# Performance work log

Measured on AMD Instinct MI355X. Metric: run time of the kernel, lower is better.

The kernel has to match this reference:

```python
import jax, jax.numpy as jnp
import numpy as np

N_NODES = 20000
N_EDGES = 320000
IN_F = 256
HID = 64
OUT_F = 64
EDGE_F = 16
HEADS = 4
NUM_CLASSES = 10
NUM_GRAPHS = 40
ALPHA = 0.2  # LeakyReLU negative slope


def _xavier(key, shape):
    fan_in, fan_out = shape[0], shape[-1]
    std = 1.414 * np.sqrt(2.0 / (fan_in + fan_out))
    return jax.random.normal(key, shape, dtype=jnp.float32) * std


def setup_inputs() -> dict:
    key = jax.random.key(0)
    ks = jax.random.split(key, 12)
    x = jax.random.normal(ks[0], (N_NODES, IN_F), dtype=jnp.float32)
    edge_index = jax.random.randint(ks[1], (2, N_EDGES), 0, N_NODES, dtype=jnp.int32)
    edge_attr = jax.random.uniform(ks[2], (N_EDGES, EDGE_F), dtype=jnp.float32)
    batch = jnp.sort(jax.random.randint(ks[3], (N_NODES,), 0, NUM_GRAPHS, dtype=jnp.int32))
    # layer 0: in=IN_F, heads=HEADS, out=HID, concat
    W0 = _xavier(ks[4], (IN_F, HEADS * HID))
    a0 = _xavier(ks[5], (HEADS, 2 * HID + EDGE_F))
    # layer 1: in=HID*HEADS, heads=HEADS, out=HID, concat
    W1 = _xavier(ks[6], (HID * HEADS, HEADS * HID))
    a1 = _xavier(ks[7], (HEADS, 2 * HID + EDGE_F))
    # layer 2: in=HID*HEADS, heads=1, out=OUT_F, mean over heads
    W2 = _xavier(ks[8], (HID * HEADS, 1 * OUT_F))
    a2 = _xavier(ks[9], (1, 2 * OUT_F + EDGE_F))
    cls_w = _xavier(ks[10], (OUT_F, NUM_CLASSES))
    cls_b = jnp.zeros((NUM_CLASSES,), dtype=jnp.float32)
    return {"x": x, "edge_index": edge_index, "edge_attr": edge_attr, "batch": batch,
            "W0": W0, "a0": a0, "W1": W1, "a1": a1, "W2": W2, "a2": a2,
            "cls_w": cls_w, "cls_b": cls_b}


def gat_layer(h, W, a, edge_index, edge_attr, heads, out_f, concat):
    n = h.shape[0]
    Wh = (h @ W).reshape(n, heads, out_f)              # [N,H,D]
    src, dst = edge_index[0], edge_index[1]
    a_i, a_j, a_e = a[:, :out_f], a[:, out_f:2 * out_f], a[:, 2 * out_f:]
    # per-node head scores, gathered per edge (equivalent to concat + dot with a)
    s_i = jnp.einsum('nhd,hd->nh', Wh, a_i)            # [N,H]
    s_j = jnp.einsum('nhd,hd->nh', Wh, a_j)            # [N,H]
    s_e = edge_attr @ a_e.T                            # [E,H]
    e = s_i[src] + s_j[dst] + s_e                      # [E,H]
    e = jnp.where(e > 0, e, ALPHA * e)                 # LeakyReLU
    # NB: faithful to source — softmax over the HEADS dim (dim=1), not per-node
    att = jax.nn.softmax(e, axis=1)                    # [E,H]
    msg = att[:, :, None] * Wh[dst]                    # [E,H,D]
    h_prime = jax.ops.segment_sum(msg, src, num_segments=n)  # scatter-add to src
    if concat:
        return jax.nn.elu(h_prime.reshape(n, heads * out_f))
    return h_prime.mean(axis=1)


def reference(x, edge_index, edge_attr, batch, W0, a0, W1, a1, W2, a2, cls_w, cls_b):
    h = gat_layer(x, W0, a0, edge_index, edge_attr, HEADS, HID, True)
    h = gat_layer(h, W1, a1, edge_index, edge_attr, HEADS, HID, True)
    h = gat_layer(h, W2, a2, edge_index, edge_attr, 1, OUT_F, False)
    # global mean pool over graphs
    sums = jax.ops.segment_sum(h, batch, num_segments=NUM_GRAPHS)
    cnts = jax.ops.segment_sum(jnp.ones((h.shape[0],), h.dtype), batch, num_segments=NUM_GRAPHS)
    pooled = sums / jnp.maximum(cnts, 1.0)[:, None]
    logits = pooled @ cls_w + cls_b
    return jax.nn.log_softmax(logits, axis=1)
```

## Files before the change

### kernel.cpp

```cpp
#include <hip/hip_runtime.h>
#include <hip/hip_bf16.h>
#include <math.h>

#define N_NODES 20000
#define N_EDGES 320000
#define IN_F 256
#define HID 64
#define HEADS 4
#define OUT_F 64
#define EDGE_F 16
#define NUM_CLASSES 10
#define NUM_GRAPHS 40
#define LRELU_ALPHA 0.2f

typedef short bf16x8 __attribute__((ext_vector_type(8)));
typedef unsigned short u16x8 __attribute__((ext_vector_type(8)));
typedef float f32x4 __attribute__((ext_vector_type(4)));

static __device__ __forceinline__ float bf2f(unsigned short u) {
    union { unsigned int i; float f; } v; v.i = ((unsigned int)u) << 16; return v.f;
}
static __device__ __forceinline__ unsigned short f2bf(float f) {
    union { float f; unsigned int i; } v; v.f = f;
    unsigned int r = v.i + 0x7FFF + ((v.i >> 16) & 1);
    return (unsigned short)(r >> 16);
}
static __device__ __forceinline__ float eluf(float a) {
    return a > 0.f ? a : __expf(a) - 1.0f;
}

__global__ void wconv_kernel(const float* __restrict__ W0, const float* __restrict__ W1,
                             const float* __restrict__ W2, unsigned short* __restrict__ W0b,
                             unsigned short* __restrict__ W1b, unsigned short* __restrict__ W2b) {
    int i = blockIdx.x * blockDim.x + threadIdx.x;
    const float* src; unsigned short* dst; int off;
    if (i < 16384)      { src = W0; dst = W0b; off = i; }
    else if (i < 32768) { src = W1; dst = W1b; off = i - 16384; }
    else if (i < 36864) { src = W2; dst = W2b; off = i - 32768; }
    else return;
    float4 v = ((const float4*)src)[off];
    ushort4 o;
    o.x = f2bf(v.x); o.y = f2bf(v.y); o.z = f2bf(v.z); o.w = f2bf(v.w);
    ((ushort4*)dst)[off] = o;
}

__global__ void count_kernel(const int* __restrict__ src, int* __restrict__ cnt) {
    int e = blockIdx.x * blockDim.x + threadIdx.x;
    if (e < N_EDGES) atomicAdd(&cnt[src[e]], 1);
}

__global__ __launch_bounds__(1024) void scan_kernel(const int* __restrict__ cnt,
                                                    int* __restrict__ row_ptr,
                                                    int* __restrict__ cursor) {
    __shared__ int wsum[16];
    __shared__ int carry_s;
    int t = threadIdx.x;
    int lane = t & 63, wave = t >> 6;
    if (t == 0) { carry_s = 0; row_ptr[0] = 0; }
    __syncthreads();
    for (int base = 0; base < N_NODES; base += 1024) {
        int idx = base + t;
        int x0 = (idx < N_NODES) ? cnt[idx] : 0;
        int x = x0;
#pragma unroll
        for (int off = 1; off < 64; off <<= 1) {
            int y = __shfl_up(x, off, 64);
            if (lane >= off) x += y;
        }
        if (lane == 63) wsum[wave] = x;
        __syncthreads();
        if (wave == 0 && lane < 16) {
            int s = wsum[lane];
#pragma unroll
            for (int off = 1; off < 16; off <<= 1) {
                int y = __shfl_up(s, off, 64);
                if (lane >= off) s += y;
            }
            wsum[lane] = s;
        }
        __syncthreads();
        int waveoff = (wave > 0) ? wsum[wave - 1] : 0;
        int carry = carry_s;
        if (idx < N_NODES) {
            int incl = x + waveoff + carry;
            row_ptr[idx + 1] = incl;
            cursor[idx] = incl - x0;
        }
        __syncthreads();
        if (t == 0) carry_s = carry + wsum[15];
        __syncthreads();
    }
}

__global__ void scatter_kernel(const int* __restrict__ src, const int* __restrict__ dst,
                               const float* __restrict__ ea, int* __restrict__ cursor,
                               int* __restrict__ srcp, int* __restrict__ dstp,
                               float* __restrict__ eap) {
    int e = blockIdx.x * blockDim.x + threadIdx.x;
    if (e < N_EDGES) {
        int s = src[e];
        int pos = atomicAdd(&cursor[s], 1);
        srcp[pos] = s;
        dstp[pos] = dst[e];
#pragma unroll
        for (int k = 0; k < 4; ++k)
            ((float4*)(eap + (size_t)pos * 16))[k] = ((const float4*)(ea + (size_t)e * 16))[k];
    }
}

template <bool AF32, bool SCORES>
__global__ __launch_bounds__(256) void gemm_bf16(const void* __restrict__ Aptr,
                                                 const unsigned short* __restrict__ B,
                                                 unsigned short* __restrict__ C,
                                                 const float* __restrict__ avec,
                                                 float* __restrict__ si, float* __restrict__ sj,
                                                 int M, int N, int K) {
    __shared__ unsigned short As[64][40];
    __shared__ unsigned short Bs[64][40];
    __shared__ unsigned short Cs[64][72];
    __shared__ float sa[128];
    int tid = threadIdx.x;
    if (SCORES && tid < 128) sa[tid] = avec[blockIdx.y * 144 + tid];
    int bm = blockIdx.x * 64, bn = blockIdx.y * 64;
    int w = tid >> 6, l = tid & 63;
    int wr = (w >> 1) * 32, wc = (w & 1) * 32;
    int lr = l & 15, lk = (l >> 4) * 8;
    f32x4 acc[2][2] = {};
    int ar = tid >> 2, akc = (tid & 3) * 8;
    int bk = tid >> 3, bn8 = tid & 7, bnc = bn8 * 8;

    for (int k0 = 0; k0 < K; k0 += 32) {
        bf16x8 av = {};
        if (bm + ar < M) {
            if constexpr (AF32) {
                const float* Af = (const float*)Aptr + (size_t)(bm + ar) * K + k0 + akc;
                float4 f0 = *(const float4*)Af;
                float4 f1 = *(const float4*)(Af + 4);
                av[0] = (short)f2bf(f0.x); av[1] = (short)f2bf(f0.y);
                av[2] = (short)f2bf(f0.z); av[3] = (short)f2bf(f0.w);
                av[4] = (short)f2bf(f1.x); av[5] = (short)f2bf(f1.y);
                av[6] = (short)f2bf(f1.z); av[7] = (short)f2bf(f1.w);
            } else {
                av = *(const bf16x8*)((const unsigned short*)Aptr + (size_t)(bm + ar) * K + k0 + akc);
            }
        }
        *(bf16x8*)&As[ar][akc] = av;
        bf16x8 bv = *(const bf16x8*)(B + (size_t)(k0 + bk) * N + bn + bnc);
#pragma unroll
        for (int j = 0; j < 8; ++j) {
            int jj = (j + bn8) & 7;
            Bs[bnc + jj][bk] = (unsigned short)bv[jj];
        }
        __syncthreads();
        bf16x8 a0 = *(const bf16x8*)&As[wr + lr][lk];
        bf16x8 a1 = *(const bf16x8*)&As[wr + 16 + lr][lk];
        bf16x8 b0 = *(const bf16x8*)&Bs[wc + lr][lk];
        bf16x8 b1 = *(const bf16x8*)&Bs[wc + 16 + lr][lk];
        acc[0][0] = __builtin_amdgcn_mfma_f32_16x16x32_bf16(a0, b0, acc[0][0], 0, 0, 0);
        acc[0][1] = __builtin_amdgcn_mfma_f32_16x16x32_bf16(a0, b1, acc[0][1], 0, 0, 0);
        acc[1][0] = __builtin_amdgcn_mfma_f32_16x16x32_bf16(a1, b0, acc[1][0], 0, 0, 0);
        acc[1][1] = __builtin_amdgcn_mfma_f32_16x16x32_bf16(a1, b1, acc[1][1], 0, 0, 0);
        __syncthreads();
    }
#pragma unroll
    for (int i = 0; i < 2; ++i)
#pragma unroll
        for (int j = 0; j < 2; ++j)
#pragma unroll
            for (int r = 0; r < 4; ++r)
                Cs[wr + i * 16 + (l >> 4) * 4 + r][wc + j * 16 + (l & 15)] = f2bf(acc[i][j][r]);
    __syncthreads();
    int row = tid >> 3, cc = (tid & 7) * 8;
#pragma unroll
    for (int p = 0; p < 2; ++p, row += 32) {
        if (bm + row < M) {
            bf16x8 o = *(const bf16x8*)&Cs[row][cc];
            *(bf16x8*)(C + (size_t)(bm + row) * N + bn + cc) = o;
        }
    }
    if (SCORES) {
        int r = tid >> 2, qq = tid & 3;
        float s0 = 0.f, s1 = 0.f;
#pragma unroll
        for (int k = 0; k < 16; ++k) {
            float f = bf2f(Cs[r][qq * 16 + k]);
            s0 += f * sa[qq * 16 + k];
            s1 += f * sa[64 + qq * 16 + k];
        }
        s0 += __shfl_xor(s0, 1, 64); s0 += __shfl_xor(s0, 2, 64);
        s1 += __shfl_xor(s1, 1, 64); s1 += __shfl_xor(s1, 2, 64);
        if (qq == 0 && bm + r < M) {
            si[(size_t)(bm + r) * 4 + blockIdx.y] = s0;
            sj[(size_t)(bm + r) * 4 + blockIdx.y] = s1;
        }
    }
}

__global__ void att_kernel(const int* __restrict__ srcp, const int* __restrict__ dstp,
                           const float* __restrict__ eap, const float* __restrict__ a,
                           const float* __restrict__ si, const float* __restrict__ sj,
                           float* __restrict__ attp) {
    __shared__ float ae[HEADS][EDGE_F];
    int tid = threadIdx.x;
    if (tid < HEADS * EDGE_F) ae[tid >> 4][tid & 15] = a[(tid >> 4) * 144 + 128 + (tid & 15)];
    __syncthreads();
    int i = blockIdx.x * blockDim.x + tid;
    if (i >= N_EDGES) return;
    int s = srcp[i], u = dstp[i];
    float4 siv = ((const float4*)si)[s];
    float4 sjv = ((const float4*)sj)[u];
    float x[16];
#pragma unroll
    for (int k = 0; k < 16; k += 4) {
        float4 v = *(const float4*)(eap + (size_t)i * 16 + k);
        x[k] = v.x; x[k + 1] = v.y; x[k + 2] = v.z; x[k + 3] = v.w;
    }
    float se0 = 0.f, se1 = 0.f, se2 = 0.f, se3 = 0.f;
#pragma unroll
    for (int k = 0; k < 16; ++k) {
        se0 += x[k] * ae[0][k];
        se1 += x[k] * ae[1][k];
        se2 += x[k] * ae[2][k];
        se3 += x[k] * ae[3][k];
    }
    float t0 = siv.x + sjv.x + se0;
    float t1 = siv.y + sjv.y + se1;
    float t2 = siv.z + sjv.z + se2;
    float t3 = siv.w + sjv.w + se3;
    t0 = t0 > 0.f ? t0 : LRELU_ALPHA * t0;
    t1 = t1 > 0.f ? t1 : LRELU_ALPHA * t1;
    t2 = t2 > 0.f ? t2 : LRELU_ALPHA * t2;
    t3 = t3 > 0.f ? t3 : LRELU_ALPHA * t3;
    float m = fmaxf(fmaxf(t0, t1), fmaxf(t2, t3));
    float p0 = __expf(t0 - m), p1 = __expf(t1 - m), p2 = __expf(t2 - m), p3 = __expf(t3 - m);
    float inv = 1.0f / (p0 + p1 + p2 + p3);
    ((float4*)attp)[i] = make_float4(p0 * inv, p1 * inv, p2 * inv, p3 * inv);
}

__global__ __launch_bounds__(256) void edge_agg_concat(
    const unsigned short* __restrict__ Whb, const float* __restrict__ attp,
    const int* __restrict__ row_ptr, const int* __restrict__ dstp,
    unsigned short* __restrict__ out) {
    int v = blockIdx.x * 4 + (threadIdx.x >> 6);
    if (v >= N_NODES) return;
    int l = threadIdx.x & 63;
    int slot = l >> 4, p = l & 15;
    int beg = row_ptr[v], end = row_ptr[v + 1];
    float acc0[8] = {}, acc1[8] = {};
    int i = beg + slot;
    int u_n = 0;
    float4 at_n = make_float4(0.f, 0.f, 0.f, 0.f);
    if (i < end) { u_n = dstp[i]; at_n = ((const float4*)attp)[i]; }
    for (; i < end; i += 4) {
        int u = u_n;
        float4 at4 = at_n;
        if (i + 4 < end) { u_n = dstp[i + 4]; at_n = ((const float4*)attp)[i + 4]; }
        const unsigned short* row = Whb + (size_t)u * 256;
        u16x8 w0 = *(const u16x8*)(row + p * 8);
        u16x8 w1 = *(const u16x8*)(row + 128 + p * 8);
        float atA = (p & 8) ? at4.y : at4.x;
        float atB = (p & 8) ? at4.w : at4.z;
#pragma unroll
        for (int j = 0; j < 8; ++j) acc0[j] += atA * bf2f(w0[j]);
#pragma unroll
        for (int j = 0; j < 8; ++j) acc1[j] += atB * bf2f(w1[j]);
    }
#pragma unroll
    for (int j = 0; j < 8; ++j) {
        acc0[j] += __shfl_xor(acc0[j], 16, 64);
        acc0[j] += __shfl_xor(acc0[j], 32, 64);
        acc1[j] += __shfl_xor(acc1[j], 16, 64);
        acc1[j] += __shfl_xor(acc1[j], 32, 64);
    }
    if (slot == 0) {
        u16x8 o0, o1;
#pragma unroll
        for (int j = 0; j < 8; ++j) {
            o0[j] = f2bf(eluf(acc0[j]));
            o1[j] = f2bf(eluf(acc1[j]));
        }
        *(u16x8*)(out + (size_t)v * 256 + p * 8) = o0;
        *(u16x8*)(out + (size_t)v * 256 + 128 + p * 8) = o1;
    }
}

__global__ __launch_bounds__(256) void edge_agg_single(
    const unsigned short* __restrict__ Whb, const int* __restrict__ row_ptr,
    const int* __restrict__ dstp, float* __restrict__ out) {
    int v = blockIdx.x * 4 + (threadIdx.x >> 6);
    if (v >= N_NODES) return;
    int l = threadIdx.x & 63;
    int slot = l >> 3, p = l & 7;
    int beg = row_ptr[v], end = row_ptr[v + 1];
    float acc[8] = {};
    int i = beg + slot;
    int u_n = 0;
    if (i < end) u_n = dstp[i];
    for (; i < end; i += 8) {
        int u = u_n;
        if (i + 8 < end) u_n = dstp[i + 8];
        u16x8 w = *(const u16x8*)(Whb + (size_t)u * 64 + p * 8);
#pragma unroll
        for (int j = 0; j < 8; ++j) acc[j] += bf2f(w[j]);
    }
#pragma unroll
    for (int j = 0; j < 8; ++j) {
        acc[j] += __shfl_xor(acc[j], 8, 64);
        acc[j] += __shfl_xor(acc[j], 16, 64);
        acc[j] += __shfl_xor(acc[j], 32, 64);
    }
    if (l < 8) {
        float4 o0 = make_float4(acc[0], acc[1], acc[2], acc[3]);
        float4 o1 = make_float4(acc[4], acc[5], acc[6], acc[7]);
        *(float4*)(out + (size_t)v * 64 + p * 8) = o0;
        *(float4*)(out + (size_t)v * 64 + p * 8 + 4) = o1;
    }
}

__global__ __launch_bounds__(1024) void pool_kernel(const float* __restrict__ h3,
                                                    const int* __restrict__ batch,
                                                    float* __restrict__ pooled) {
    int g = blockIdx.x;
    int lane = threadIdx.x & 63;
    int wave = threadIdx.x >> 6;
    int lo = 0, hi = N_NODES;
    while (lo < hi) { int mid = (lo + hi) >> 1; if (batch[mid] < g) lo = mid + 1; else hi = mid; }
    int start = lo;
    lo = start; hi = N_NODES;
    while (lo < hi) { int mid = (lo + hi) >> 1; if (batch[mid] < g + 1) lo = mid + 1; else hi = mid; }
    int endi = lo;
    float s = 0.f;
    for (int v = start + wave; v < endi; v += 16) s += h3[(size_t)v * 64 + lane];
    __shared__ float red[16][64];
    red[wave][lane] = s;
    __syncthreads();
    if (wave == 0) {
        float t = red[0][lane];
#pragma unroll
        for (int w = 1; w < 16; ++w) t += red[w][lane];
        float c = (float)((endi - start) > 1 ? (endi - start) : 1);
        pooled[g * 64 + lane] = t / c;
    }
}

__global__ void classify_kernel(const float* __restrict__ pooled, const float* __restrict__ cw,
                                const float* __restrict__ cb, float* __restrict__ out) {
    int g = threadIdx.x;
    if (g >= NUM_GRAPHS) return;
    float lg[NUM_CLASSES];
#pragma unroll
    for (int c = 0; c < NUM_CLASSES; ++c) lg[c] = cb[c];
    for (int d = 0; d < OUT_F; ++d) {
        float p = pooled[g * 64 + d];
#pragma unroll
        for (int c = 0; c < NUM_CLASSES; ++c) lg[c] += p * cw[d * NUM_CLASSES + c];
    }
    float m = lg[0];
#pragma unroll
    for (int c = 1; c < NUM_CLASSES; ++c) m = fmaxf(m, lg[c]);
    float s = 0.f;
#pragma unroll
    for (int c = 0; c < NUM_CLASSES; ++c) s += expf(lg[c] - m);
    float lse = m + logf(s);
#pragma unroll
    for (int c = 0; c < NUM_CLASSES; ++c) out[g * NUM_CLASSES + c] = lg[c] - lse;
}

extern "C" void kernel_launch(void* const* d_in, const int* in_sizes, int n_in,
                              void* d_out, int out_size, void* d_ws, size_t ws_size,
                              hipStream_t stream) {
    const float* x   = (const float*)d_in[0];
    const int*   ei  = (const int*)d_in[1];
    const float* ea  = (const float*)d_in[2];
    const int* batch = (const int*)d_in[3];
    const float* W0  = (const float*)d_in[4];
    const float* a0  = (const float*)d_in[5];
    const float* W1  = (const float*)d_in[6];
    const float* a1  = (const float*)d_in[7];
    const float* W2  = (const float*)d_in[8];
    const float* cw  = (const float*)d_in[10];
    const float* cb  = (const float*)d_in[11];
    float* out = (float*)d_out;

    const int* srcg = ei;
    const int* dstg = ei + N_EDGES;

    char* ws = (char*)d_ws;
    size_t off = 0;
    auto alloc = [&](size_t bytes) -> char* {
        char* p = ws + off;
        off += (bytes + 255) & ~(size_t)255;
        return p;
    };
    unsigned short* W0b  = (unsigned short*)alloc(256 * 256 * 2);
    unsigned short* W1b  = (unsigned short*)alloc(256 * 256 * 2);
    unsigned short* W2b  = (unsigned short*)alloc(256 * 64 * 2);
    unsigned short* Whb  = (unsigned short*)alloc((size_t)N_NODES * 256 * 2);
    unsigned short* hAb  = (unsigned short*)alloc((size_t)N_NODES * 256 * 2);
    unsigned short* hBb  = (unsigned short*)alloc((size_t)N_NODES * 256 * 2);
    unsigned short* Wh2b = (unsigned short*)alloc((size_t)N_NODES * 64 * 2);
    float* si   = (float*)alloc((size_t)N_NODES * HEADS * 4);
    float* sj   = (float*)alloc((size_t)N_NODES * HEADS * 4);
    float* attp = (float*)alloc((size_t)N_EDGES * HEADS * 4);
    float* eap  = (float*)alloc((size_t)N_EDGES * EDGE_F * 4);
    int* row_ptr = (int*)alloc((N_NODES + 1) * 4);
    int* cursor  = (int*)alloc(N_NODES * 4);
    int* cnt  = (int*)alloc(N_NODES * 4);
    int* srcp = (int*)alloc(N_EDGES * 4);
    int* dstp = (int*)alloc(N_EDGES * 4);
    float* h3 = (float*)alloc((size_t)N_NODES * 64 * 4);
    float* pooled = (float*)alloc(NUM_GRAPHS * 64 * 4);

    wconv_kernel<<<144, 256, 0, stream>>>(W0, W1, W2, W0b, W1b, W2b);

    hipMemsetAsync(cnt, 0, N_NODES * 4, stream);
    count_kernel<<<(N_EDGES + 255) / 256, 256, 0, stream>>>(srcg, cnt);
    scan_kernel<<<1, 1024, 0, stream>>>(cnt, row_ptr, cursor);
    scatter_kernel<<<(N_EDGES + 255) / 256, 256, 0, stream>>>(srcg, dstg, ea, cursor,
                                                              srcp, dstp, eap);

    dim3 ggrid((N_NODES + 63) / 64, 4);
    dim3 ggrid2((N_NODES + 63) / 64, 1);
    int atb = (N_EDGES + 255) / 256;
    int agb = (N_NODES + 3) / 4;

    gemm_bf16<true, true><<<ggrid, 256, 0, stream>>>(x, W0b, Whb, a0, si, sj, N_NODES, 256, 256);
    att_kernel<<<atb, 256, 0, stream>>>(srcp, dstp, eap, a0, si, sj, attp);
    edge_agg_concat<<<agb, 256, 0, stream>>>(Whb, attp, row_ptr, dstp, hAb);

    gemm_bf16<false, true><<<ggrid, 256, 0, stream>>>(hAb, W1b, Whb, a1, si, sj, N_NODES, 256, 256);
    att_kernel<<<atb, 256, 0, stream>>>(srcp, dstp, eap, a1, si, sj, attp);
    edge_agg_concat<<<agb, 256, 0, stream>>>(Whb, attp, row_ptr, dstp, hBb);

    gemm_bf16<false, false><<<ggrid2, 256, 0, stream>>>(hBb, W2b, Wh2b, nullptr, nullptr, nullptr,
                                                        N_NODES, 64, 256);
    edge_agg_single<<<agb, 256, 0, stream>>>(Wh2b, row_ptr, dstp, h3);

    pool_kernel<<<NUM_GRAPHS, 1024, 0, stream>>>(h3, batch, pooled);
    classify_kernel<<<1, 64, 0, stream>>>(pooled, cw, cb, out);
}
```

Baseline: 209.3 us.

## Fuse attention into edge aggregation, precompute edge scores, enlarge GEMM tile

The separate attention kernel is removed. Edge-feature scores for both layers are computed once in the scatter pass and stored per edge as four floats. The LeakyReLU and head softmax are computed inline inside edge_agg_concat. This drops the 16-float permuted edge-attribute buffer, the srcp array and two kernel launches. Separately, the GEMM tile grows to 128 rows with each wave covering all 64 columns, and the count memset is folded into the weight-conversion kernel. The risks are fewer GEMM blocks and an extra dependent gather of sj per edge in the aggregation loop.

```diff
diff --git a/kernel.cpp b/kernel.cpp
--- a/kernel.cpp
+++ b/kernel.cpp
@@ -29,19 +29,25 @@
     return a > 0.f ? a : __expf(a) - 1.0f;
 }
 
-__global__ void wconv_kernel(const float* __restrict__ W0, const float* __restrict__ W1,
-                             const float* __restrict__ W2, unsigned short* __restrict__ W0b,
-                             unsigned short* __restrict__ W1b, unsigned short* __restrict__ W2b) {
-    int i = blockIdx.x * blockDim.x + threadIdx.x;
-    const float* src; unsigned short* dst; int off;
-    if (i < 16384)      { src = W0; dst = W0b; off = i; }
-    else if (i < 32768) { src = W1; dst = W1b; off = i - 16384; }
-    else if (i < 36864) { src = W2; dst = W2b; off = i - 32768; }
-    else return;
-    float4 v = ((const float4*)src)[off];
-    ushort4 o;
-    o.x = f2bf(v.x); o.y = f2bf(v.y); o.z = f2bf(v.z); o.w = f2bf(v.w);
-    ((ushort4*)dst)[off] = o;
+__global__ void prep_kernel(const float* __restrict__ W0, const float* __restrict__ W1,
+                            const float* __restrict__ W2, unsigned short* __restrict__ W0b,
+                            unsigned short* __restrict__ W1b, unsigned short* __restrict__ W2b,
+                            int* __restrict__ cnt) {
+    int b = blockIdx.x;
+    if (b < 144) {
+        int i = b * 256 + threadIdx.x;
+        const float* src; unsigned short* dst; int off;
+        if (i < 16384)      { src = W0; dst = W0b; off = i; }
+        else if (i < 32768) { src = W1; dst = W1b; off = i - 16384; }
+        else                { src = W2; dst = W2b; off = i - 32768; }
+        float4 v = ((const float4*)src)[off];
+        ushort4 o;
+        o.x = f2bf(v.x); o.y = f2bf(v.y); o.z = f2bf(v.z); o.w = f2bf(v.w);
+        ((ushort4*)dst)[off] = o;
+    } else {
+        int j = (b - 144) * 256 + threadIdx.x;
+        if (j < N_NODES / 4) ((int4*)cnt)[j] = make_int4(0, 0, 0, 0);
+    }
 }
 
 __global__ void count_kernel(const int* __restrict__ src, int* __restrict__ cnt) {
@@ -93,19 +99,36 @@
 }
 
 __global__ void scatter_kernel(const int* __restrict__ src, const int* __restrict__ dst,
-                               const float* __restrict__ ea, int* __restrict__ cursor,
-                               int* __restrict__ srcp, int* __restrict__ dstp,
-                               float* __restrict__ eap) {
-    int e = blockIdx.x * blockDim.x + threadIdx.x;
-    if (e < N_EDGES) {
-        int s = src[e];
-        int pos = atomicAdd(&cursor[s], 1);
-        srcp[pos] = s;
-        dstp[pos] = dst[e];
-#pragma unroll
-        for (int k = 0; k < 4; ++k)
-            ((float4*)(eap + (size_t)pos * 16))[k] = ((const float4*)(ea + (size_t)e * 16))[k];
-    }
+                               const float* __restrict__ ea, const float* __restrict__ a0,
+                               const float* __restrict__ a1, int* __restrict__ cursor,
+                               int* __restrict__ dstp, float* __restrict__ se0,
+                               float* __restrict__ se1) {
+    __shared__ float ae[2][4][16];
+    int tid = threadIdx.x;
+    if (tid < 64) ae[0][tid >> 4][tid & 15] = a0[(tid >> 4) * 144 + 128 + (tid & 15)];
+    else if (tid < 128) { int t = tid - 64; ae[1][t >> 4][t & 15] = a1[(t >> 4) * 144 + 128 + (t & 15)]; }
+    __syncthreads();
+    int e = blockIdx.x * blockDim.x + tid;
+    if (e >= N_EDGES) return;
+    int s = src[e];
+    int pos = atomicAdd(&cursor[s], 1);
+    dstp[pos] = dst[e];
+    float x[16];
+#pragma unroll
+    for (int k = 0; k < 16; k += 4) {
+        float4 v = *(const float4*)(ea + (size_t)e * 16 + k);
+        x[k] = v.x; x[k + 1] = v.y; x[k + 2] = v.z; x[k + 3] = v.w;
+    }
+    float4 o0 = make_float4(0.f, 0.f, 0.f, 0.f), o1 = o0;
+#pragma unroll
+    for (int k = 0; k < 16; ++k) {
+        o0.x += x[k] * ae[0][0][k]; o0.y += x[k] * ae[0][1][k];
+        o0.z += x[k] * ae[0][2][k]; o0.w += x[k] * ae[0][3][k];
+        o1.x += x[k] * ae[1][0][k]; o1.y += x[k] * ae[1][1][k];
+        o1.z += x[k] * ae[1][2][k]; o1.w += x[k] * ae[1][3][k];
+    }
+    ((float4*)se0)[pos] = o0;
+    ((float4*)se1)[pos] = o1;
 }
 
 template <bool AF32, bool SCORES>
@@ -115,36 +138,45 @@
                                                  const float* __restrict__ avec,
                                                  float* __restrict__ si, float* __restrict__ sj,
                                                  int M, int N, int K) {
-    __shared__ unsigned short As[64][40];
+    __shared__ unsigned short As[128][40];
     __shared__ unsigned short Bs[64][40];
-    __shared__ unsigned short Cs[64][72];
+    __shared__ unsigned short Cs[128][72];
     __shared__ float sa[128];
     int tid = threadIdx.x;
     if (SCORES && tid < 128) sa[tid] = avec[blockIdx.y * 144 + tid];
-    int bm = blockIdx.x * 64, bn = blockIdx.y * 64;
+    int bm = blockIdx.x * 128, bn = blockIdx.y * 64;
     int w = tid >> 6, l = tid & 63;
-    int wr = (w >> 1) * 32, wc = (w & 1) * 32;
+    int wr = w * 32;
     int lr = l & 15, lk = (l >> 4) * 8;
-    f32x4 acc[2][2] = {};
-    int ar = tid >> 2, akc = (tid & 3) * 8;
+    f32x4 acc[2][4] = {};
+    int ar = tid >> 1, akc = (tid & 1) * 16;
     int bk = tid >> 3, bn8 = tid & 7, bnc = bn8 * 8;
 
     for (int k0 = 0; k0 < K; k0 += 32) {
-        bf16x8 av = {};
+        bf16x8 av0 = {}, av1 = {};
         if (bm + ar < M) {
             if constexpr (AF32) {
                 const float* Af = (const float*)Aptr + (size_t)(bm + ar) * K + k0 + akc;
-                float4 f0 = *(const float4*)Af;
-                float4 f1 = *(const float4*)(Af + 4);
-                av[0] = (short)f2bf(f0.x); av[1] = (short)f2bf(f0.y);
-                av[2] = (short)f2bf(f0.z); av[3] = (short)f2bf(f0.w);
-                av[4] = (short)f2bf(f1.x); av[5] = (short)f2bf(f1.y);
-                av[6] = (short)f2bf(f1.z); av[7] = (short)f2bf(f1.w);
+                float4 f0 = ((const float4*)Af)[0];
+                float4 f1 = ((const float4*)Af)[1];
+                float4 f2 = ((const float4*)Af)[2];
+                float4 f3 = ((const float4*)Af)[3];
+                av0[0] = (short)f2bf(f0.x); av0[1] = (short)f2bf(f0.y);
+                av0[2] = (short)f2bf(f0.z); av0[3] = (short)f2bf(f0.w);
+                av0[4] = (short)f2bf(f1.x); av0[5] = (short)f2bf(f1.y);
+                av0[6] = (short)f2bf(f1.z); av0[7] = (short)f2bf(f1.w);
+                av1[0] = (short)f2bf(f2.x); av1[1] = (short)f2bf(f2.y);
+                av1[2] = (short)f2bf(f2.z); av1[3] = (short)f2bf(f2.w);
+                av1[4] = (short)f2bf(f3.x); av1[5] = (short)f2bf(f3.y);
+                av1[6] = (short)f2bf(f3.z); av1[7] = (short)f2bf(f3.w);
             } else {
-                av = *(const bf16x8*)((const unsigned short*)Aptr + (size_t)(bm + ar) * K + k0 + akc);
+                const unsigned short* Ab = (const unsigned short*)Aptr + (size_t)(bm + ar) * K + k0 + akc;
+                av0 = *(const bf16x8*)Ab;
+                av1 = *(const bf16x8*)(Ab + 8);
             }
         }
-        *(bf16x8*)&As[ar][akc] = av;
+        *(bf16x8*)&As[ar][akc] = av0;
+        *(bf16x8*)&As[ar][akc + 8] = av1;
         bf16x8 bv = *(const bf16x8*)(B + (size_t)(k0 + bk) * N + bn + bnc);
 #pragma unroll
         for (int j = 0; j < 8; ++j) {
@@ -154,91 +186,59 @@
         __syncthreads();
         bf16x8 a0 = *(const bf16x8*)&As[wr + lr][lk];
         bf16x8 a1 = *(const bf16x8*)&As[wr + 16 + lr][lk];
-        bf16x8 b0 = *(const bf16x8*)&Bs[wc + lr][lk];
-        bf16x8 b1 = *(const bf16x8*)&Bs[wc + 16 + lr][lk];
+        bf16x8 b0 = *(const bf16x8*)&Bs[lr][lk];
+        bf16x8 b1 = *(const bf16x8*)&Bs[16 + lr][lk];
+        bf16x8 b2 = *(const bf16x8*)&Bs[32 + lr][lk];
+        bf16x8 b3 = *(const bf16x8*)&Bs[48 + lr][lk];
         acc[0][0] = __builtin_amdgcn_mfma_f32_16x16x32_bf16(a0, b0, acc[0][0], 0, 0, 0);
         acc[0][1] = __builtin_amdgcn_mfma_f32_16x16x32_bf16(a0, b1, acc[0][1], 0, 0, 0);
+        acc[0][2] = __builtin_amdgcn_mfma_f32_16x16x32_bf16(a0, b2, acc[0][2], 0, 0, 0);
+        acc[0][3] = __builtin_amdgcn_mfma_f32_16x16x32_bf16(a0, b3, acc[0][3], 0, 0, 0);
         acc[1][0] = __builtin_amdgcn_mfma_f32_16x16x32_bf16(a1, b0, acc[1][0], 0, 0, 0);
         acc[1][1] = __builtin_amdgcn_mfma_f32_16x16x32_bf16(a1, b1, acc[1][1], 0, 0, 0);
+        acc[1][2] = __builtin_amdgcn_mfma_f32_16x16x32_bf16(a1, b2, acc[1][2], 0, 0, 0);
+        acc[1][3] = __builtin_amdgcn_mfma_f32_16x16x32_bf16(a1, b3, acc[1][3], 0, 0, 0);
         __syncthreads();
     }
 #pragma unroll
     for (int i = 0; i < 2; ++i)
 #pragma unroll
-        for (int j = 0; j < 2; ++j)
+        for (int j = 0; j < 4; ++j)
 #pragma unroll
             for (int r = 0; r < 4; ++r)
-                Cs[wr + i * 16 + (l >> 4) * 4 + r][wc + j * 16 + (l & 15)] = f2bf(acc[i][j][r]);
+                Cs[wr + i * 16 + (l >> 4) * 4 + r][j * 16 + (l & 15)] = f2bf(acc[i][j][r]);
     __syncthreads();
-    int row = tid >> 3, cc = (tid & 7) * 8;
-#pragma unroll
-    for (int p = 0; p < 2; ++p, row += 32) {
-        if (bm + row < M) {
-            bf16x8 o = *(const bf16x8*)&Cs[row][cc];
-            *(bf16x8*)(C + (size_t)(bm + row) * N + bn + cc) = o;
+    {
+        int row = tid >> 3, cc = (tid & 7) * 8;
+#pragma unroll
+        for (int p = 0; p < 4; ++p, row += 32) {
+            if (bm + row < M) {
+                bf16x8 o = *(const bf16x8*)&Cs[row][cc];
+                *(bf16x8*)(C + (size_t)(bm + row) * N + bn + cc) = o;
+            }
         }
     }
     if (SCORES) {
-        int r = tid >> 2, qq = tid & 3;
+        int r = tid >> 1, half = tid & 1;
         float s0 = 0.f, s1 = 0.f;
 #pragma unroll
-        for (int k = 0; k < 16; ++k) {
-            float f = bf2f(Cs[r][qq * 16 + k]);
-            s0 += f * sa[qq * 16 + k];
-            s1 += f * sa[64 + qq * 16 + k];
-        }
-        s0 += __shfl_xor(s0, 1, 64); s0 += __shfl_xor(s0, 2, 64);
-        s1 += __shfl_xor(s1, 1, 64); s1 += __shfl_xor(s1, 2, 64);
-        if (qq == 0 && bm + r < M) {
+        for (int k = 0; k < 32; ++k) {
+            float f = bf2f(Cs[r][half * 32 + k]);
+            s0 += f * sa[half * 32 + k];
+            s1 += f * sa[64 + half * 32 + k];
+        }
+        s0 += __shfl_xor(s0, 1, 64);
+        s1 += __shfl_xor(s1, 1, 64);
+        if (half == 0 && bm + r < M) {
             si[(size_t)(bm + r) * 4 + blockIdx.y] = s0;
             sj[(size_t)(bm + r) * 4 + blockIdx.y] = s1;
         }
     }
 }
 
-__global__ void att_kernel(const int* __restrict__ srcp, const int* __restrict__ dstp,
-                           const float* __restrict__ eap, const float* __restrict__ a,
-                           const float* __restrict__ si, const float* __restrict__ sj,
-                           float* __restrict__ attp) {
-    __shared__ float ae[HEADS][EDGE_F];
-    int tid = threadIdx.x;
-    if (tid < HEADS * EDGE_F) ae[tid >> 4][tid & 15] = a[(tid >> 4) * 144 + 128 + (tid & 15)];
-    __syncthreads();
-    int i = blockIdx.x * blockDim.x + tid;
-    if (i >= N_EDGES) return;
-    int s = srcp[i], u = dstp[i];
-    float4 siv = ((const float4*)si)[s];
-    float4 sjv = ((const float4*)sj)[u];
-    float x[16];
-#pragma unroll
-    for (int k = 0; k < 16; k += 4) {
-        float4 v = *(const float4*)(eap + (size_t)i * 16 + k);
-        x[k] = v.x; x[k + 1] = v.y; x[k + 2] = v.z; x[k + 3] = v.w;
-    }
-    float se0 = 0.f, se1 = 0.f, se2 = 0.f, se3 = 0.f;
-#pragma unroll
-    for (int k = 0; k < 16; ++k) {
-        se0 += x[k] * ae[0][k];
-        se1 += x[k] * ae[1][k];
-        se2 += x[k] * ae[2][k];
-        se3 += x[k] * ae[3][k];
-    }
-    float t0 = siv.x + sjv.x + se0;
-    float t1 = siv.y + sjv.y + se1;
-    float t2 = siv.z + sjv.z + se2;
-    float t3 = siv.w + sjv.w + se3;
-    t0 = t0 > 0.f ? t0 : LRELU_ALPHA * t0;
-    t1 = t1 > 0.f ? t1 : LRELU_ALPHA * t1;
-    t2 = t2 > 0.f ? t2 : LRELU_ALPHA * t2;
-    t3 = t3 > 0.f ? t3 : LRELU_ALPHA * t3;
-    float m = fmaxf(fmaxf(t0, t1), fmaxf(t2, t3));
-    float p0 = __expf(t0 - m), p1 = __expf(t1 - m), p2 = __expf(t2 - m), p3 = __expf(t3 - m);
-    float inv = 1.0f / (p0 + p1 + p2 + p3);
-    ((float4*)attp)[i] = make_float4(p0 * inv, p1 * inv, p2 * inv, p3 * inv);
-}
-
 __global__ __launch_bounds__(256) void edge_agg_concat(
-    const unsigned short* __restrict__ Whb, const float* __restrict__ attp,
+    const unsigned short* __restrict__ Whb, const float* __restrict__ sev,
+    const float* __restrict__ si, const float* __restrict__ sj,
     const int* __restrict__ row_ptr, const int* __restrict__ dstp,
     unsigned short* __restrict__ out) {
     int v = blockIdx.x * 4 + (threadIdx.x >> 6);
@@ -246,20 +246,40 @@
     int l = threadIdx.x & 63;
     int slot = l >> 4, p = l & 15;
     int beg = row_ptr[v], end = row_ptr[v + 1];
+    float4 si4 = ((const float4*)si)[v];
     float acc0[8] = {}, acc1[8] = {};
     int i = beg + slot;
     int u_n = 0;
-    float4 at_n = make_float4(0.f, 0.f, 0.f, 0.f);
-    if (i < end) { u_n = dstp[i]; at_n = ((const float4*)attp)[i]; }
+    float4 se_n = make_float4(0.f, 0.f, 0.f, 0.f), sj_n = se_n;
+    if (i < end) {
+        u_n = dstp[i];
+        se_n = ((const float4*)sev)[i];
+        sj_n = ((const float4*)sj)[u_n];
+    }
     for (; i < end; i += 4) {
         int u = u_n;
-        float4 at4 = at_n;
-        if (i + 4 < end) { u_n = dstp[i + 4]; at_n = ((const float4*)attp)[i + 4]; }
+        float4 se4 = se_n, sj4 = sj_n;
+        if (i + 4 < end) {
+            u_n = dstp[i + 4];
+            se_n = ((const float4*)sev)[i + 4];
+            sj_n = ((const float4*)sj)[u_n];
+        }
+        float t0 = si4.x + sj4.x + se4.x;
+        float t1 = si4.y + sj4.y + se4.y;
+        float t2 = si4.z + sj4.z + se4.z;
+        float t3 = si4.w + sj4.w + se4.w;
+        t0 = t0 > 0.f ? t0 : LRELU_ALPHA * t0;
+        t1 = t1 > 0.f ? t1 : LRELU_ALPHA * t1;
+        t2 = t2 > 0.f ? t2 : LRELU_ALPHA * t2;
+        t3 = t3 > 0.f ? t3 : LRELU_ALPHA * t3;
+        float m = fmaxf(fmaxf(t0, t1), fmaxf(t2, t3));
+        float p0 = __expf(t0 - m), p1 = __expf(t1 - m), p2 = __expf(t2 - m), p3 = __expf(t3 - m);
+        float inv = 1.0f / (p0 + p1 + p2 + p3);
         const unsigned short* row = Whb + (size_t)u * 256;
         u16x8 w0 = *(const u16x8*)(row + p * 8);
         u16x8 w1 = *(const u16x8*)(row + 128 + p * 8);
-        float atA = (p & 8) ? at4.y : at4.x;
-        float atB = (p & 8) ? at4.w : at4.z;
+        float atA = ((p & 8) ? p1 : p0) * inv;
+        float atB = ((p & 8) ? p3 : p2) * inv;
 #pragma unroll
         for (int j = 0; j < 8; ++j) acc0[j] += atA * bf2f(w0[j]);
 #pragma unroll
@@ -401,36 +421,31 @@
     unsigned short* Wh2b = (unsigned short*)alloc((size_t)N_NODES * 64 * 2);
     float* si   = (float*)alloc((size_t)N_NODES * HEADS * 4);
     float* sj   = (float*)alloc((size_t)N_NODES * HEADS * 4);
-    float* attp = (float*)alloc((size_t)N_EDGES * HEADS * 4);
-    float* eap  = (float*)alloc((size_t)N_EDGES * EDGE_F * 4);
+    float* se0  = (float*)alloc((size_t)N_EDGES * HEADS * 4);
+    float* se1  = (float*)alloc((size_t)N_EDGES * HEADS * 4);
     int* row_ptr = (int*)alloc((N_NODES + 1) * 4);
     int* cursor  = (int*)alloc(N_NODES * 4);
     int* cnt  = (int*)alloc(N_NODES * 4);
-    int* srcp = (int*)alloc(N_EDGES * 4);
     int* dstp = (int*)alloc(N_EDGES * 4);
     float* h3 = (float*)alloc((size_t)N_NODES * 64 * 4);
     float* pooled = (float*)alloc(NUM_GRAPHS * 64 * 4);
 
-    wconv_kernel<<<144, 256, 0, stream>>>(W0, W1, W2, W0b, W1b, W2b);
-
-    hipMemsetAsync(cnt, 0, N_NODES * 4, stream);
+    prep_kernel<<<144 + (N_NODES / 4 + 255) / 256, 256, 0, stream>>>(W0, W1, W2, W0b, W1b, W2b, cnt);
+
     count_kernel<<<(N_EDGES + 255) / 256, 256, 0, stream>>>(srcg, cnt);
     scan_kernel<<<1, 1024, 0, stream>>>(cnt, row_ptr, cursor);
-    scatter_kernel<<<(N_EDGES + 255) / 256, 256, 0, stream>>>(srcg, dstg, ea, cursor,
-                                                              srcp, dstp, eap);
-
-    dim3 ggrid((N_NODES + 63) / 64, 4);
-    dim3 ggrid2((N_NODES + 63) / 64, 1);
-    int atb = (N_EDGES + 255) / 256;
+    scatter_kernel<<<(N_EDGES + 255) / 256, 256, 0, stream>>>(srcg, dstg, ea, a0, a1, cursor,
+                                                              dstp, se0, se1);
+
+    dim3 ggrid((N_NODES + 127) / 128, 4);
+    dim3 ggrid2((N_NODES + 127) / 128, 1);
     int agb = (N_NODES + 3) / 4;
 
     gemm_bf16<true, true><<<ggrid, 256, 0, stream>>>(x, W0b, Whb, a0, si, sj, N_NODES, 256, 256);
-    att_kernel<<<atb, 256, 0, stream>>>(srcp, dstp, eap, a0, si, sj, attp);
-    edge_agg_concat<<<agb, 256, 0, stream>>>(Whb, attp, row_ptr, dstp, hAb);
+    edge_agg_concat<<<agb, 256, 0, stream>>>(Whb, se0, si, sj, row_ptr, dstp, hAb);
 
     gemm_bf16<false, true><<<ggrid, 256, 0, stream>>>(hAb, W1b, Whb, a1, si, sj, N_NODES, 256, 256);
-    att_kernel<<<atb, 256, 0, stream>>>(srcp, dstp, eap, a1, si, sj, attp);
-    edge_agg_concat<<<agb, 256, 0, stream>>>(Whb, attp, row_ptr, dstp, hBb);
+    edge_agg_concat<<<agb, 256, 0, stream>>>(Whb, se1, si, sj, row_ptr, dstp, hBb);
 
     gemm_bf16<false, false><<<ggrid2, 256, 0, stream>>>(hBb, W2b, Wh2b, nullptr, nullptr, nullptr,
                                                         N_NODES, 64, 256);
```

After: 207.8 us. About the same (-0.7%).
